# Performance work log

Hardware: AMD Instinct MI355X
Metric: run time of the kernel (lower is better)

## Reference

```python
import jax, jax.numpy as jnp
import numpy as np

N_NODES = 100000
N_EDGES = 3200000


def gcn_conv(x, edge_index, W, b, n_nodes):
    # PyG GCNConv: x' = D^{-1/2} (A + I) D^{-1/2} (x W) + b
    h = x @ W  # [N, C_out]
    loop = jnp.arange(n_nodes, dtype=edge_index.dtype)
    src = jnp.concatenate([edge_index[0], loop])  # source nodes j
    dst = jnp.concatenate([edge_index[1], loop])  # target nodes i (aggregation)
    deg = jax.ops.segment_sum(jnp.ones_like(dst, h.dtype), dst, num_segments=n_nodes)
    dinv = jnp.where(deg > 0, jax.lax.rsqrt(deg), 0.0)
    norm = dinv[src] * dinv[dst]  # [E+N]
    msg = h[src] * norm[:, None]  # gather + scale
    out = jax.ops.segment_sum(msg, dst, num_segments=n_nodes)  # scatter-add
    return out + b


def setup_inputs() -> dict:
    key = jax.random.key(0)
    ks = jax.random.split(key, 6)
    x = jax.random.normal(ks[0], (N_NODES, 1), dtype=jnp.float32)
    edge_index = jax.random.randint(ks[1], (2, N_EDGES), 0, N_NODES, dtype=jnp.int64)
    W1 = jax.random.normal(ks[2], (1, 16), dtype=jnp.float32) * (1.0 / np.sqrt(1))
    b1 = jnp.zeros((16,), dtype=jnp.float32)
    W2 = jax.random.normal(ks[3], (16, 16), dtype=jnp.float32) * (1.0 / np.sqrt(16))
    b2 = jnp.zeros((16,), dtype=jnp.float32)
    Wl = jax.random.normal(ks[4], (16, 1), dtype=jnp.float32) * (1.0 / np.sqrt(16))
    bl = jnp.zeros((1,), dtype=jnp.float32)
    return {"x": x, "edge_index": edge_index, "W1": W1, "b1": b1,
            "W2": W2, "b2": b2, "Wl": Wl, "bl": bl}


def reference(x, edge_index, W1, b1, W2, b2, Wl, bl):
    n = x.shape[0]
    h = gcn_conv(x, edge_index, W1, b1, n)
    h = jax.nn.relu(h)
    # F.dropout(training=self.training): identity in eval mode
    h = gcn_conv(h, edge_index, W2, b2, n)
    return h @ Wl + bl  # [N, 1]
```

## Files before the change

### kernel.cpp

```cpp
#include <hip/hip_runtime.h>

#define N_NODES  100000
#define N_EDGES  3200000
#define NB       8
#define BN       12544
#define S1       96
#define G1       (NB * S1)
#define SA       32
#define GA       (NB * SA)
#define RPB      (S1 / SA)
#define THR      512
#define THRA     1024
#define SLICE    33336
#define CAP_BLK  5120


__global__ __launch_bounds__(THR, 6) void k_degpart(
        const int* __restrict__ src, const int* __restrict__ dstp,
        unsigned* __restrict__ cnt, unsigned* __restrict__ pedge,
        unsigned short* __restrict__ cnt16) {
    __shared__ unsigned facc[BN];
    __shared__ unsigned cur;
    const int tid = threadIdx.x, lane = tid & 63;
    const int bu = blockIdx.x / S1, sub = blockIdx.x % S1;
    for (int i = tid; i < BN; i += THR) facc[i] = 0u;
    if (tid == 0) cur = 0;
    __syncthreads();

    const unsigned base_node = (unsigned)bu * BN;
    unsigned* reg = pedge + (size_t)blockIdx.x * CAP_BLK;
    const uint4* s4 = (const uint4*)src;
    const uint4* d4 = (const uint4*)dstp;
    const int e0 = sub * SLICE;
    const int qbeg = e0 >> 2;
    const int qlim = (e0 + SLICE < N_EDGES ? e0 + SLICE : N_EDGES) >> 2;

    for (int q = qbeg + tid; q < qlim; q += THR) {
        const uint4 dv = d4[q], sv = s4[q];
        const unsigned dd[4] = { dv.x, dv.y, dv.z, dv.w };
        const unsigned ss[4] = { sv.x, sv.y, sv.z, sv.w };
        #pragma unroll
        for (int k = 0; k < 4; ++k) {
            const unsigned d = dd[k];
            const unsigned dl = d - base_node;
            const bool in = (d / BN) == (unsigned)bu;
            if (in) atomicAdd(&facc[dl], 1u);
            const unsigned long long m = __ballot(in);
            const unsigned pos = (unsigned)__popcll(m & ((1ull << lane) - 1ull));
            unsigned b0 = 0;
            if (lane == 0) b0 = atomicAdd(&cur, (unsigned)__popcll(m));
            b0 = __shfl(b0, 0, 64);
            if (in) {
                const unsigned slot = b0 + pos;
                if (slot < CAP_BLK) reg[slot] = ss[k] | (dl << 17);
            }
        }
    }
    __syncthreads();
    if (tid == 0) cnt[blockIdx.x] = cur < CAP_BLK ? cur : CAP_BLK;
    unsigned short* po = cnt16 + (size_t)blockIdx.x * BN;
    for (int i = tid; i < BN; i += THR) po[i] = (unsigned short)facc[i];
}

__global__ __launch_bounds__(THR) void k_red1(const float* __restrict__ x,
        const unsigned short* __restrict__ cnt16,
        float* __restrict__ dinv, float* __restrict__ xs) {
    const int g = blockIdx.x * THR + threadIdx.x;
    if (g >= N_NODES) return;
    const int bu = g / BN, l = g - bu * BN;
    const unsigned short* pp = cnt16 + (size_t)(bu * S1) * BN + l;
    unsigned run = 0;
    #pragma unroll 8
    for (int s = 0; s < S1; ++s) run += pp[(size_t)s * BN];
    const float di = rsqrtf((float)run + 1.f);
    dinv[g] = di;
    xs[g] = x[g] * di;
}

__global__ __launch_bounds__(THRA) void k_acc(
        const unsigned* __restrict__ pedge, const unsigned* __restrict__ cnt,
        const float* __restrict__ vals, float* __restrict__ partials) {
    __shared__ float facc[BN];
    const int tid = threadIdx.x;
    const int bu = blockIdx.x / SA, sub = blockIdx.x % SA;
    for (int i = tid; i < BN; i += THRA) facc[i] = 0.f;
    __syncthreads();
    #pragma unroll
    for (int r3 = 0; r3 < RPB; ++r3) {
        const int r = bu * S1 + sub * RPB + r3;
        const unsigned n = cnt[r];
        const unsigned* reg = pedge + (size_t)r * CAP_BLK;
        for (unsigned j = tid; j < n; j += THRA) {
            const unsigned w = reg[j];
            atomicAdd(&facc[w >> 17], vals[w & 0x1FFFFu]);
        }
    }
    __syncthreads();
    float* po = partials + (size_t)blockIdx.x * BN;
    for (int i = tid; i < BN; i += THRA) po[i] = facc[i];
}

__device__ __forceinline__ float sum_partials(const float* __restrict__ partials,
                                              int g) {
    const int bu = g / BN, l = g - bu * BN;
    const float* pp = partials + (size_t)(bu * SA) * BN + l;
    float s = 0.f;
    #pragma unroll
    for (int k = 0; k < SA; ++k) s += pp[(size_t)k * BN];
    return s;
}

__global__ __launch_bounds__(THR) void k_red2(const float* __restrict__ x,
        const float* __restrict__ partials, const float* __restrict__ dinv,
        const float* __restrict__ W1, const float* __restrict__ b1,
        const float* __restrict__ W2, const float* __restrict__ Wl,
        float* __restrict__ us, float* __restrict__ uself) {
    const int g = blockIdx.x * THR + threadIdx.x;
    if (g >= N_NODES) return;
    const float sum = sum_partials(partials, g);
    const float di = dinv[g];
    const float s1 = di * sum + x[g] * di * di;
    float u = 0.f;
    #pragma unroll
    for (int c = 0; c < 16; ++c) {
        float vcc = 0.f;
        #pragma unroll
        for (int k = 0; k < 16; ++k) vcc += W2[c * 16 + k] * Wl[k];
        u += fmaxf(W1[c] * s1 + b1[c], 0.f) * vcc;
    }
    us[g] = u * di;
    uself[g] = u * di * di;
}

__global__ __launch_bounds__(THR) void k_red3(const float* __restrict__ partials,
        const float* __restrict__ dinv, const float* __restrict__ uself,
        const float* __restrict__ W2, const float* __restrict__ b2,
        const float* __restrict__ Wl, const float* __restrict__ bl,
        float* __restrict__ out) {
    const int g = blockIdx.x * THR + threadIdx.x;
    if (g >= N_NODES) return;
    const float sum = sum_partials(partials, g);
    float vcb = bl[0];
    #pragma unroll
    for (int c = 0; c < 16; ++c) {
        float vcc = 0.f;
        #pragma unroll
        for (int k = 0; k < 16; ++k) vcc += W2[c * 16 + k] * Wl[k];
        vcb += b2[c] * vcc;
    }
    out[g] = dinv[g] * sum + uself[g] + vcb;
}

extern "C" void kernel_launch(void* const* d_in, const int* in_sizes, int n_in,
                              void* d_out, int out_size, void* d_ws, size_t ws_size,
                              hipStream_t stream) {
    const float* x  = (const float*)d_in[0];
    const int*   ei = (const int*)d_in[1];
    const float* W1 = (const float*)d_in[2];
    const float* b1 = (const float*)d_in[3];
    const float* W2 = (const float*)d_in[4];
    const float* b2 = (const float*)d_in[5];
    const float* Wl = (const float*)d_in[6];
    const float* bl = (const float*)d_in[7];
    float* out = (float*)d_out;

    const int* src  = ei;
    const int* dstp = ei + N_EDGES;

    unsigned* cnt         = (unsigned*)d_ws;
    unsigned* pedge       = cnt + 1024;
    unsigned short* cnt16 = (unsigned short*)(pedge + (size_t)G1 * CAP_BLK);
    float*    partials    = (float*)(cnt16 + (size_t)G1 * BN);
    float*    dinv        = partials + (size_t)GA * BN;
    float*    xs          = dinv + N_NODES;
    float*    us          = xs + N_NODES;
    float*    uself       = us + N_NODES;

    const int red_blocks = (N_NODES + THR - 1) / THR;

    k_degpart<<<G1, THR, 0, stream>>>(src, dstp, cnt, pedge, cnt16);
    k_red1<<<red_blocks, THR, 0, stream>>>(x, cnt16, dinv, xs);
    k_acc<<<GA, THRA, 0, stream>>>(pedge, cnt, xs, partials);
    k_red2<<<red_blocks, THR, 0, stream>>>(x, partials, dinv, W1, b1, W2, Wl, us, uself);
    k_acc<<<GA, THRA, 0, stream>>>(pedge, cnt, us, partials);
    k_red3<<<red_blocks, THR, 0, stream>>>(partials, dinv, uself, W2, b2, Wl, bl, out);
}
```

Baseline: 172.6 us.

## Partition edges in a single pass into per-block bucket regions, count degrees separately

Replaces the degree-and-partition kernel, where each bucket's blocks rescanned the full edge list, with a single pass that scatters each edge into one of seven per-block bucket regions using ballot-based compaction. Degree counting moves to a new shared-memory accumulation kernel over the packed edges. Buckets become power-of-two sized so index math uses shifts. This removes repeated edge-list reads at the cost of more ballot work per edge, an extra kernel launch, and a tight per-bucket capacity that may silently drop edges on overflow.

```diff
diff --git a/kernel.cpp b/kernel.cpp
--- a/kernel.cpp
+++ b/kernel.cpp
@@ -2,107 +2,131 @@
 
 #define N_NODES  100000
 #define N_EDGES  3200000
-#define NB       8
-#define BN       12544
-#define S1       96
-#define G1       (NB * S1)
+#define NB       7
+#define BSH      14
+#define BN       16384
+#define PBLK     512
+#define PTHR     512
+#define PSLICE   6272
+#define CAP_SB   1152
 #define SA       32
 #define GA       (NB * SA)
-#define RPB      (S1 / SA)
-#define THR      512
-#define THRA     1024
-#define SLICE    33336
-#define CAP_BLK  5120
-
-
-__global__ __launch_bounds__(THR, 6) void k_degpart(
-        const int* __restrict__ src, const int* __restrict__ dstp,
-        unsigned* __restrict__ cnt, unsigned* __restrict__ pedge,
-        unsigned short* __restrict__ cnt16) {
-    __shared__ unsigned facc[BN];
-    __shared__ unsigned cur;
+#define ATHR     1024
+#define PPB      (PBLK / SA)
+#define RTHR     512
+
+
+__global__ __launch_bounds__(PTHR) void k_part(const int* __restrict__ src,
+        const int* __restrict__ dstp, unsigned* __restrict__ cnt,
+        unsigned* __restrict__ pedge) {
+    __shared__ unsigned curs[NB];
     const int tid = threadIdx.x, lane = tid & 63;
-    const int bu = blockIdx.x / S1, sub = blockIdx.x % S1;
-    for (int i = tid; i < BN; i += THR) facc[i] = 0u;
-    if (tid == 0) cur = 0;
-    __syncthreads();
-
-    const unsigned base_node = (unsigned)bu * BN;
-    unsigned* reg = pedge + (size_t)blockIdx.x * CAP_BLK;
+    if (tid < NB) curs[tid] = 0;
+    __syncthreads();
+    const int e0 = blockIdx.x * PSLICE;
+    const int qbeg = e0 >> 2;
+    int qend = (e0 + PSLICE) >> 2;
+    const int qmax = N_EDGES >> 2;
+    if (qend > qmax) qend = qmax;
     const uint4* s4 = (const uint4*)src;
     const uint4* d4 = (const uint4*)dstp;
-    const int e0 = sub * SLICE;
-    const int qbeg = e0 >> 2;
-    const int qlim = (e0 + SLICE < N_EDGES ? e0 + SLICE : N_EDGES) >> 2;
-
-    for (int q = qbeg + tid; q < qlim; q += THR) {
-        const uint4 dv = d4[q], sv = s4[q];
+    unsigned* myped = pedge + (size_t)blockIdx.x * NB * CAP_SB;
+
+    for (int q = qbeg + tid; q < qend; q += PTHR) {
+        const uint4 sv = s4[q], dv = d4[q];
+        const unsigned ss[4] = { sv.x, sv.y, sv.z, sv.w };
         const unsigned dd[4] = { dv.x, dv.y, dv.z, dv.w };
-        const unsigned ss[4] = { sv.x, sv.y, sv.z, sv.w };
         #pragma unroll
         for (int k = 0; k < 4; ++k) {
-            const unsigned d = dd[k];
-            const unsigned dl = d - base_node;
-            const bool in = (d / BN) == (unsigned)bu;
-            if (in) atomicAdd(&facc[dl], 1u);
-            const unsigned long long m = __ballot(in);
-            const unsigned pos = (unsigned)__popcll(m & ((1ull << lane) - 1ull));
-            unsigned b0 = 0;
-            if (lane == 0) b0 = atomicAdd(&cur, (unsigned)__popcll(m));
-            b0 = __shfl(b0, 0, 64);
-            if (in) {
-                const unsigned slot = b0 + pos;
-                if (slot < CAP_BLK) reg[slot] = ss[k] | (dl << 17);
+            const unsigned b = dd[k] >> BSH;
+            const unsigned w = ss[k] | ((dd[k] & (BN - 1u)) << 17);
+            #pragma unroll
+            for (unsigned bb = 0; bb < NB; ++bb) {
+                const unsigned long long m = __ballot(b == bb);
+                if (m) {
+                    const int ldr = __ffsll((long long)m) - 1;
+                    unsigned base = 0;
+                    if (lane == ldr)
+                        base = atomicAdd(&curs[bb], (unsigned)__popcll(m));
+                    base = __shfl(base, ldr, 64);
+                    if (b == bb) {
+                        const unsigned pos =
+                            (unsigned)__popcll(m & ((1ull << lane) - 1ull));
+                        const unsigned slot = base + pos;
+                        if (slot < CAP_SB) myped[bb * CAP_SB + slot] = w;
+                    }
+                }
             }
         }
     }
     __syncthreads();
-    if (tid == 0) cnt[blockIdx.x] = cur < CAP_BLK ? cur : CAP_BLK;
-    unsigned short* po = cnt16 + (size_t)blockIdx.x * BN;
-    for (int i = tid; i < BN; i += THR) po[i] = (unsigned short)facc[i];
-}
-
-__global__ __launch_bounds__(THR) void k_red1(const float* __restrict__ x,
-        const unsigned short* __restrict__ cnt16,
+    if (tid < NB) {
+        unsigned c = curs[tid];
+        cnt[blockIdx.x * NB + tid] = c < CAP_SB ? c : CAP_SB;
+    }
+}
+
+__global__ __launch_bounds__(ATHR) void k_degacc(const unsigned* __restrict__ pedge,
+        const unsigned* __restrict__ cnt, unsigned short* __restrict__ p16) {
+    __shared__ unsigned facc[BN];
+    const int tid = threadIdx.x;
+    const int bu = blockIdx.x / SA, sub = blockIdx.x % SA;
+    for (int i = tid; i < BN; i += ATHR) facc[i] = 0u;
+    __syncthreads();
+    #pragma unroll
+    for (int r = 0; r < PPB; ++r) {
+        const int pb = sub * PPB + r;
+        const unsigned n = cnt[pb * NB + bu];
+        const unsigned* reg = pedge + ((size_t)pb * NB + bu) * CAP_SB;
+        for (unsigned j = tid; j < n; j += ATHR)
+            atomicAdd(&facc[reg[j] >> 17], 1u);
+    }
+    __syncthreads();
+    unsigned short* po = p16 + (size_t)blockIdx.x * BN;
+    for (int i = tid; i < BN; i += ATHR) po[i] = (unsigned short)facc[i];
+}
+
+__global__ __launch_bounds__(RTHR) void k_red1(const float* __restrict__ x,
+        const unsigned short* __restrict__ p16,
         float* __restrict__ dinv, float* __restrict__ xs) {
-    const int g = blockIdx.x * THR + threadIdx.x;
+    const int g = blockIdx.x * RTHR + threadIdx.x;
     if (g >= N_NODES) return;
-    const int bu = g / BN, l = g - bu * BN;
-    const unsigned short* pp = cnt16 + (size_t)(bu * S1) * BN + l;
+    const int bu = g >> BSH, l = g & (BN - 1);
+    const unsigned short* pp = p16 + (size_t)(bu * SA) * BN + l;
     unsigned run = 0;
-    #pragma unroll 8
-    for (int s = 0; s < S1; ++s) run += pp[(size_t)s * BN];
+    #pragma unroll
+    for (int s = 0; s < SA; ++s) run += pp[(size_t)s * BN];
     const float di = rsqrtf((float)run + 1.f);
     dinv[g] = di;
     xs[g] = x[g] * di;
 }
 
-__global__ __launch_bounds__(THRA) void k_acc(
-        const unsigned* __restrict__ pedge, const unsigned* __restrict__ cnt,
-        const float* __restrict__ vals, float* __restrict__ partials) {
+__global__ __launch_bounds__(ATHR) void k_acc(const unsigned* __restrict__ pedge,
+        const unsigned* __restrict__ cnt, const float* __restrict__ vals,
+        float* __restrict__ partials) {
     __shared__ float facc[BN];
     const int tid = threadIdx.x;
     const int bu = blockIdx.x / SA, sub = blockIdx.x % SA;
-    for (int i = tid; i < BN; i += THRA) facc[i] = 0.f;
-    __syncthreads();
-    #pragma unroll
-    for (int r3 = 0; r3 < RPB; ++r3) {
-        const int r = bu * S1 + sub * RPB + r3;
-        const unsigned n = cnt[r];
-        const unsigned* reg = pedge + (size_t)r * CAP_BLK;
-        for (unsigned j = tid; j < n; j += THRA) {
+    for (int i = tid; i < BN; i += ATHR) facc[i] = 0.f;
+    __syncthreads();
+    #pragma unroll
+    for (int r = 0; r < PPB; ++r) {
+        const int pb = sub * PPB + r;
+        const unsigned n = cnt[pb * NB + bu];
+        const unsigned* reg = pedge + ((size_t)pb * NB + bu) * CAP_SB;
+        for (unsigned j = tid; j < n; j += ATHR) {
             const unsigned w = reg[j];
             atomicAdd(&facc[w >> 17], vals[w & 0x1FFFFu]);
         }
     }
     __syncthreads();
     float* po = partials + (size_t)blockIdx.x * BN;
-    for (int i = tid; i < BN; i += THRA) po[i] = facc[i];
+    for (int i = tid; i < BN; i += ATHR) po[i] = facc[i];
 }
 
 __device__ __forceinline__ float sum_partials(const float* __restrict__ partials,
                                               int g) {
-    const int bu = g / BN, l = g - bu * BN;
+    const int bu = g >> BSH, l = g & (BN - 1);
     const float* pp = partials + (size_t)(bu * SA) * BN + l;
     float s = 0.f;
     #pragma unroll
@@ -110,12 +134,12 @@
     return s;
 }
 
-__global__ __launch_bounds__(THR) void k_red2(const float* __restrict__ x,
+__global__ __launch_bounds__(RTHR) void k_red2(const float* __restrict__ x,
         const float* __restrict__ partials, const float* __restrict__ dinv,
         const float* __restrict__ W1, const float* __restrict__ b1,
         const float* __restrict__ W2, const float* __restrict__ Wl,
         float* __restrict__ us, float* __restrict__ uself) {
-    const int g = blockIdx.x * THR + threadIdx.x;
+    const int g = blockIdx.x * RTHR + threadIdx.x;
     if (g >= N_NODES) return;
     const float sum = sum_partials(partials, g);
     const float di = dinv[g];
@@ -132,12 +156,12 @@
     uself[g] = u * di * di;
 }
 
-__global__ __launch_bounds__(THR) void k_red3(const float* __restrict__ partials,
+__global__ __launch_bounds__(RTHR) void k_red3(const float* __restrict__ partials,
         const float* __restrict__ dinv, const float* __restrict__ uself,
         const float* __restrict__ W2, const float* __restrict__ b2,
         const float* __restrict__ Wl, const float* __restrict__ bl,
         float* __restrict__ out) {
-    const int g = blockIdx.x * THR + threadIdx.x;
+    const int g = blockIdx.x * RTHR + threadIdx.x;
     if (g >= N_NODES) return;
     const float sum = sum_partials(partials, g);
     float vcb = bl[0];
@@ -168,20 +192,21 @@
     const int* dstp = ei + N_EDGES;
 
     unsigned* cnt         = (unsigned*)d_ws;
-    unsigned* pedge       = cnt + 1024;
-    unsigned short* cnt16 = (unsigned short*)(pedge + (size_t)G1 * CAP_BLK);
-    float*    partials    = (float*)(cnt16 + (size_t)G1 * BN);
+    unsigned* pedge       = cnt + 4096;
+    unsigned short* p16   = (unsigned short*)(pedge + (size_t)PBLK * NB * CAP_SB);
+    float*    partials    = (float*)(p16 + (size_t)GA * BN);
     float*    dinv        = partials + (size_t)GA * BN;
     float*    xs          = dinv + N_NODES;
     float*    us          = xs + N_NODES;
     float*    uself       = us + N_NODES;
 
-    const int red_blocks = (N_NODES + THR - 1) / THR;
-
-    k_degpart<<<G1, THR, 0, stream>>>(src, dstp, cnt, pedge, cnt16);
-    k_red1<<<red_blocks, THR, 0, stream>>>(x, cnt16, dinv, xs);
-    k_acc<<<GA, THRA, 0, stream>>>(pedge, cnt, xs, partials);
-    k_red2<<<red_blocks, THR, 0, stream>>>(x, partials, dinv, W1, b1, W2, Wl, us, uself);
-    k_acc<<<GA, THRA, 0, stream>>>(pedge, cnt, us, partials);
-    k_red3<<<red_blocks, THR, 0, stream>>>(partials, dinv, uself, W2, b2, Wl, bl, out);
-}
+    const int red_blocks = (N_NODES + RTHR - 1) / RTHR;
+
+    k_part<<<PBLK, PTHR, 0, stream>>>(src, dstp, cnt, pedge);
+    k_degacc<<<GA, ATHR, 0, stream>>>(pedge, cnt, p16);
+    k_red1<<<red_blocks, RTHR, 0, stream>>>(x, p16, dinv, xs);
+    k_acc<<<GA, ATHR, 0, stream>>>(pedge, cnt, xs, partials);
+    k_red2<<<red_blocks, RTHR, 0, stream>>>(x, partials, dinv, W1, b1, W2, Wl, us, uself);
+    k_acc<<<GA, ATHR, 0, stream>>>(pedge, cnt, us, partials);
+    k_red3<<<red_blocks, RTHR, 0, stream>>>(partials, dinv, uself, W2, b2, Wl, bl, out);
+}
```

After: 187.1 us. 8.4% more time.
